# Optimization experiments

Measured on AMD Instinct MI355X. Metric: run time of the kernel, lower is better.

Reference implementation:

```python
import jax, jax.numpy as jnp
import numpy as np

L2 = 65536          # edges per orientation (L=256 torus)
N = 2 * L2          # total edges
FIN = 8             # nfeatCNN_in
FOUT = 8            # nfeatCNN_out
K = 13              # kernel size (neighbor shifts per edge)
SCALE = (2.0 + 2.0 * np.e) / (np.e - 1.0)


def setup_inputs() -> dict:
    key = jax.random.key(0)
    ks = jax.random.split(key, 8)
    x = jax.random.normal(ks[0], (FIN * N,), dtype=jnp.float32)
    Wconv_hor = jax.random.normal(ks[1], (FOUT, FIN, K), dtype=jnp.float32) * 0.1
    Wconv_vert = jax.random.normal(ks[2], (FOUT, FIN, K), dtype=jnp.float32) * 0.1
    bconv_hor = jnp.zeros((FOUT,), dtype=jnp.float32)
    bconv_vert = jnp.zeros((FOUT,), dtype=jnp.float32)
    mask_hor = jax.random.randint(ks[3], (L2, FOUT, FIN, K), 0, 2).astype(bool)
    mask_vert = jax.random.randint(ks[4], (L2, FOUT, FIN, K), 0, 2).astype(bool)
    ker_hor = jax.random.randint(ks[5], (L2, K), 0, N, dtype=jnp.int32)
    ker_vert = jax.random.randint(ks[6], (L2, K), 0, N, dtype=jnp.int32)
    hor_edge_lst = jnp.arange(L2, dtype=jnp.int32)
    vert_edge_lst = jnp.arange(L2, dtype=jnp.int32) + L2
    return {
        "x": x,
        "Wconv_hor": Wconv_hor, "Wconv_vert": Wconv_vert,
        "bconv_hor": bconv_hor, "bconv_vert": bconv_vert,
        "mask_hor": mask_hor, "mask_vert": mask_vert,
        "ker_hor": ker_hor, "ker_vert": ker_vert,
        "hor_edge_lst": hor_edge_lst, "vert_edge_lst": vert_edge_lst,
    }


def reference(x, Wconv_hor, Wconv_vert, bconv_hor, bconv_vert,
              mask_hor, mask_vert, ker_hor, ker_vert,
              hor_edge_lst, vert_edge_lst):
    fout, fin, _ = Wconv_hor.shape
    n = x.shape[0] // fin
    xm = x.reshape(fin, n)                      # (fin, N)

    def branch(W, mask, ker, b):
        xg = xm[:, ker]                         # gather -> (fin, E, K)
        Wm = W[None] * mask.astype(W.dtype)     # (E, fout, fin, K)
        # per-edge masked contraction over (fin, K); vectorized over edges
        z = jnp.einsum('eoik,iek->oe', Wm, xg)  # (fout, E)
        return z + b[:, None]

    x_hor = branch(Wconv_hor, mask_hor, ker_hor, bconv_hor)
    x_vert = branch(Wconv_vert, mask_vert, ker_vert, bconv_vert)

    out = jnp.zeros((fout, n), dtype=x.dtype)
    out = out.at[:, hor_edge_lst].set(x_hor)
    out = out.at[:, vert_edge_lst].set(x_vert)
    return (jax.nn.sigmoid(out) - 0.5) * jnp.asarray(SCALE, out.dtype)
```

## Files before the change

### kernel.cpp

```cpp
#include <hip/hip_runtime.h>
#include <math.h>

#define L2C   65536
#define NC    (2 * L2C)
#define FINC  8
#define FOUTC 8
#define KC    13
#define BLOCK 256
#define EPB   4

constexpr double E_D = 2.71828182845904523536;
constexpr float SCALE_F = (float)((2.0 + 2.0 * E_D) / (E_D - 1.0));


__global__ __launch_bounds__(256)
void transpose_x_kernel(const float* __restrict__ x, float* __restrict__ xt) {
    int n = blockIdx.x * 256 + threadIdx.x;
    float v[FINC];
#pragma unroll
    for (int i = 0; i < FINC; ++i) v[i] = x[(size_t)i * NC + n];
    float4* dst = reinterpret_cast<float4*>(xt + ((size_t)n << 3));
    dst[0] = make_float4(v[0], v[1], v[2], v[3]);
    dst[1] = make_float4(v[4], v[5], v[6], v[7]);
}

__global__ __launch_bounds__(BLOCK)
void edge_conv_kernel(const float* __restrict__ xt,
                      const float* __restrict__ Wh, const float* __restrict__ Wv,
                      const float* __restrict__ bh, const float* __restrict__ bv,
                      const unsigned char* __restrict__ mh,
                      const unsigned char* __restrict__ mv,
                      const int* __restrict__ kh, const int* __restrict__ kv,
                      float* __restrict__ out)
{
    __shared__ float Wsh[FOUTC * FINC * KC];

    const int tid  = threadIdx.x;
    const int lane = tid & 63;
    const int o    = lane >> 3;
    const int i    = lane & 7;

    const int blk = blockIdx.x;
    const int blocks_per_branch = L2C / EPB;
    const bool hor = (blk < blocks_per_branch);

    const float*         W    = hor ? Wh  : Wv;
    const float*         bias = hor ? bh  : bv;
    const unsigned char* mask = hor ? mh  : mv;
    const int*           ker  = hor ? kh  : kv;
    const int bblk = hor ? blk : blk - blocks_per_branch;
    const int be   = bblk * EPB + (tid >> 6);
    const int col  = hor ? be : (be + L2C);

    for (int j = tid; j < FOUTC * FINC * KC; j += BLOCK) Wsh[j] = W[j];

    const unsigned char probe = mh[(size_t)(lane * 4 + 1)];
    const bool words = (__ballot(probe != 0) == 0ull);

    __syncthreads();

    unsigned long long myb = 0;
    if (words) {
        const unsigned int* mw = reinterpret_cast<const unsigned int*>(mask)
                                 + (size_t)be * 832 + lane;
#pragma unroll
        for (int t = 0; t < KC; ++t) {
            unsigned long long bal = __ballot(mw[t * 64] != 0u);
            if (lane == t) myb = bal;
        }
    } else {
        const unsigned char* mb = mask + (size_t)be * 832 + lane;
#pragma unroll
        for (int t = 0; t < KC; ++t) {
            unsigned long long bal = __ballot(mb[t * 64] != 0);
            if (lane == t) myb = bal;
        }
    }

    int cols[KC];
#pragma unroll
    for (int k = 0; k < KC; ++k) cols[k] = ker[(size_t)be * KC + k];

    const int s     = lane * KC;
    const int u0    = s >> 6;
    const int shift = s & 63;
    unsigned long long lo = __shfl(myb, u0);
    unsigned long long hi = __shfl(myb, u0 + 1);
    unsigned int mbits = (unsigned int)(lo >> shift);
    if (shift) mbits |= (unsigned int)(hi << (64 - shift));
    mbits &= 0x1FFFu;

    float acc = 0.0f;
#pragma unroll
    for (int k = 0; k < KC; ++k) {
        const float xv = xt[((size_t)cols[k] << 3) + i];
        const float wk = Wsh[lane * KC + k];
        const float wm = ((mbits >> k) & 1u) ? wk : 0.0f;
        acc = fmaf(wm, xv, acc);
    }

    acc += __shfl_xor(acc, 1);
    acc += __shfl_xor(acc, 2);
    acc += __shfl_xor(acc, 4);

    if (i == 0) {
        const float z   = acc + bias[o];
        const float sig = 1.0f / (1.0f + __expf(-z));
        out[(size_t)o * NC + col] = (sig - 0.5f) * SCALE_F;
    }
}

extern "C" void kernel_launch(void* const* d_in, const int* in_sizes, int n_in,
                              void* d_out, int out_size, void* d_ws, size_t ws_size,
                              hipStream_t stream) {
    const float*         x   = (const float*)d_in[0];
    const float*         Wh  = (const float*)d_in[1];
    const float*         Wv  = (const float*)d_in[2];
    const float*         bh  = (const float*)d_in[3];
    const float*         bv  = (const float*)d_in[4];
    const unsigned char* mh  = (const unsigned char*)d_in[5];
    const unsigned char* mv  = (const unsigned char*)d_in[6];
    const int*           kh  = (const int*)d_in[7];
    const int*           kv  = (const int*)d_in[8];
    float* out = (float*)d_out;
    float* xt  = (float*)d_ws;

    transpose_x_kernel<<<NC / 256, 256, 0, stream>>>(x, xt);
    edge_conv_kernel<<<NC / EPB, BLOCK, 0, stream>>>(
        xt, Wh, Wv, bh, bv, mh, mv, kh, kv, out);
}
```

Measured before the change: 452.1 us.

## Process 64 edges per block with LDS-staged mask bits and coalesced output

Each block now handles 64 edges instead of 4. Mask bits are ballot-compressed cooperatively into shared memory, and neighbor indices are staged in LDS. Weights are hoisted into registers once per thread and reused across 16 edges per wave. Results go into a shared buffer so the sigmoid output writes are contiguous per feature row rather than scattered single-lane stores. This adds LDS use and a second barrier, and reduces the number of blocks.

```diff
diff --git a/kernel.cpp b/kernel.cpp
--- a/kernel.cpp
+++ b/kernel.cpp
@@ -7,11 +7,12 @@
 #define FOUTC 8
 #define KC    13
 #define BLOCK 256
-#define EPB   4
+#define EPB   64
+#define CHUNKS (EPB * 832 / 64)
+#define CPW    (CHUNKS / 4)
 
 constexpr double E_D = 2.71828182845904523536;
 constexpr float SCALE_F = (float)((2.0 + 2.0 * E_D) / (E_D - 1.0));
-
 
 __global__ __launch_bounds__(256)
 void transpose_x_kernel(const float* __restrict__ x, float* __restrict__ xt) {
@@ -24,7 +25,7 @@
     dst[1] = make_float4(v[4], v[5], v[6], v[7]);
 }
 
-__global__ __launch_bounds__(BLOCK)
+__global__ __launch_bounds__(BLOCK, 8)
 void edge_conv_kernel(const float* __restrict__ xt,
                       const float* __restrict__ Wh, const float* __restrict__ Wv,
                       const float* __restrict__ bh, const float* __restrict__ bv,
@@ -33,10 +34,14 @@
                       const int* __restrict__ kh, const int* __restrict__ kv,
                       float* __restrict__ out)
 {
+    __shared__ unsigned long long bitbuf[CHUNKS];
     __shared__ float Wsh[FOUTC * FINC * KC];
+    __shared__ int   kersh[EPB * KC];
+    __shared__ float resbuf[FOUTC * 68];
 
     const int tid  = threadIdx.x;
     const int lane = tid & 63;
+    const int w    = tid >> 6;
     const int o    = lane >> 3;
     const int i    = lane & 7;
 
@@ -49,64 +54,73 @@
     const unsigned char* mask = hor ? mh  : mv;
     const int*           ker  = hor ? kh  : kv;
     const int bblk = hor ? blk : blk - blocks_per_branch;
-    const int be   = bblk * EPB + (tid >> 6);
-    const int col  = hor ? be : (be + L2C);
+    const int be0  = bblk * EPB;
+    const int col0 = hor ? be0 : be0 + L2C;
 
     for (int j = tid; j < FOUTC * FINC * KC; j += BLOCK) Wsh[j] = W[j];
+    for (int j = tid; j < EPB * KC; j += BLOCK) kersh[j] = ker[(size_t)be0 * KC + j];
 
     const unsigned char probe = mh[(size_t)(lane * 4 + 1)];
     const bool words = (__ballot(probe != 0) == 0ull);
 
+    if (words) {
+        const unsigned int* mw =
+            reinterpret_cast<const unsigned int*>(mask) + (size_t)be0 * 832;
+#pragma unroll 8
+        for (int t = 0; t < CPW; ++t) {
+            const int chunk = w * CPW + t;
+            unsigned int v = mw[(size_t)chunk * 64 + lane];
+            unsigned long long bal = __ballot(v != 0u);
+            if (lane == 0) bitbuf[chunk] = bal;
+        }
+    } else {
+        const unsigned char* mb = mask + (size_t)be0 * 832;
+#pragma unroll 8
+        for (int t = 0; t < CPW; ++t) {
+            const int chunk = w * CPW + t;
+            unsigned char v = mb[(size_t)chunk * 64 + lane];
+            unsigned long long bal = __ballot(v != 0);
+            if (lane == 0) bitbuf[chunk] = bal;
+        }
+    }
     __syncthreads();
 
-    unsigned long long myb = 0;
-    if (words) {
-        const unsigned int* mw = reinterpret_cast<const unsigned int*>(mask)
-                                 + (size_t)be * 832 + lane;
+    float wreg[KC];
 #pragma unroll
-        for (int t = 0; t < KC; ++t) {
-            unsigned long long bal = __ballot(mw[t * 64] != 0u);
-            if (lane == t) myb = bal;
+    for (int k = 0; k < KC; ++k) wreg[k] = Wsh[lane * KC + k];
+    const float bo = bias[o];
+
+    const unsigned int* bb32 = reinterpret_cast<const unsigned int*>(bitbuf);
+#pragma unroll 4
+    for (int e8 = 0; e8 < 16; ++e8) {
+        const int e    = w * 16 + e8;
+        const int flat = e * 832 + lane * KC;
+        const int dw   = flat >> 5;
+        const unsigned int lo32 = bb32[dw];
+        const unsigned int hi32 = bb32[dw + 1];
+        const unsigned long long both =
+            (unsigned long long)lo32 | ((unsigned long long)hi32 << 32);
+        const unsigned int mbits = (unsigned int)(both >> (flat & 31)) & 0x1FFFu;
+
+        float acc = 0.0f;
+#pragma unroll
+        for (int k = 0; k < KC; ++k) {
+            const int c    = kersh[e * KC + k];
+            const float xv = xt[((size_t)c << 3) + i];
+            acc = fmaf(((mbits >> k) & 1u) ? wreg[k] : 0.0f, xv, acc);
         }
-    } else {
-        const unsigned char* mb = mask + (size_t)be * 832 + lane;
-#pragma unroll
-        for (int t = 0; t < KC; ++t) {
-            unsigned long long bal = __ballot(mb[t * 64] != 0);
-            if (lane == t) myb = bal;
-        }
+        acc += __shfl_xor(acc, 1);
+        acc += __shfl_xor(acc, 2);
+        acc += __shfl_xor(acc, 4);
+        if (i == 0) resbuf[o * 68 + e] = acc + bo;
     }
+    __syncthreads();
 
-    int cols[KC];
-#pragma unroll
-    for (int k = 0; k < KC; ++k) cols[k] = ker[(size_t)be * KC + k];
-
-    const int s     = lane * KC;
-    const int u0    = s >> 6;
-    const int shift = s & 63;
-    unsigned long long lo = __shfl(myb, u0);
-    unsigned long long hi = __shfl(myb, u0 + 1);
-    unsigned int mbits = (unsigned int)(lo >> shift);
-    if (shift) mbits |= (unsigned int)(hi << (64 - shift));
-    mbits &= 0x1FFFu;
-
-    float acc = 0.0f;
-#pragma unroll
-    for (int k = 0; k < KC; ++k) {
-        const float xv = xt[((size_t)cols[k] << 3) + i];
-        const float wk = Wsh[lane * KC + k];
-        const float wm = ((mbits >> k) & 1u) ? wk : 0.0f;
-        acc = fmaf(wm, xv, acc);
-    }
-
-    acc += __shfl_xor(acc, 1);
-    acc += __shfl_xor(acc, 2);
-    acc += __shfl_xor(acc, 4);
-
-    if (i == 0) {
-        const float z   = acc + bias[o];
+    for (int j = tid; j < FOUTC * EPB; j += BLOCK) {
+        const int oo = j >> 6, e = j & 63;
+        const float z   = resbuf[oo * 68 + e];
         const float sig = 1.0f / (1.0f + __expf(-z));
-        out[(size_t)o * NC + col] = (sig - 0.5f) * SCALE_F;
+        out[(size_t)oo * NC + col0 + e] = (sig - 0.5f) * SCALE_F;
     }
 }
 
```

Result: slower. 500.4 us (+10.7%).
